# Kernel optimization log

Hardware: AMD Instinct MI355X
Metric: run time of the kernel (lower is better)

The kernel has to match this reference:

```python
import jax, jax.numpy as jnp
import numpy as np

N_NODES = 50000
N_EDGES = 1_600_000
F_IN = 128
F_OUT = 8
K_TAPS = 4
AVG_DEG = 32.0


def setup_inputs() -> dict:
    key = jax.random.key(0)
    k1, k2, k3, k4, k5 = jax.random.split(key, 5)
    x = jax.random.normal(k1, (N_NODES, F_IN), dtype=jnp.float32)
    gso_rows = jax.random.randint(k2, (N_EDGES,), 0, N_NODES, dtype=jnp.int32)
    gso_cols = jax.random.randint(k3, (N_EDGES,), 0, N_NODES, dtype=jnp.int32)
    gso_vals = jax.random.uniform(k4, (N_EDGES,), dtype=jnp.float32) / AVG_DEG
    # filterCoeff = randn(outFeat, filter_order) * 0.1 as in torch __init__
    coeff = jax.random.normal(k5, (F_OUT, K_TAPS), dtype=jnp.float32) * 0.1
    return {"x": x, "gso_rows": gso_rows, "gso_cols": gso_cols,
            "gso_vals": gso_vals, "coeff": coeff}


def reference(x, gso_rows, gso_cols, gso_vals, coeff):
    # Faithful to the torch code INCLUDING its carried-over SpMV state:
    # output feature o uses powers S^{1+o(K-1)} .. S^{o(K-1)+K} of x.
    F_out, K = coeff.shape
    N = x.shape[0]
    max_power = F_out * (K - 1) + 1  # highest S power needed

    def spmv(Z):  # S @ Z via edge-list gather + segment_sum scatter
        return jax.ops.segment_sum(gso_vals[:, None] * Z[gso_cols], gso_rows,
                                   num_segments=N)

    def step(Z, _):
        Zn = spmv(Z)
        return Zn, Zn.sum(axis=1)  # sum over in-features done up-front

    # s[p-1, n] = sum_f (S^p x)[n, f], for p = 1..max_power
    _, s = jax.lax.scan(step, x, None, length=max_power)  # (max_power, N)

    # power index (0-based into s) used by output o, tap i: o*(K-1) + i
    idx = jnp.arange(F_out)[:, None] * (K - 1) + jnp.arange(K)[None, :]  # (F_out, K)
    sg = s[idx]  # (F_out, K, N)
    y = jnp.einsum('ok,okn->no', coeff, sg)  # (N, F_out)
    return y
```

## Files before the change

kernel.cpp:

```cpp
#include <hip/hip_runtime.h>
#include <hip/hip_bf16.h>

#define N_NODES 50000
#define N_EDGES 1600000
#define F_IN    128
#define F_OUT   8
#define K_TAPS  4
#define MAX_POWER 25

#define NBLK    256
#define RPB     196
#define CHUNK   4096
#define NPART   391
#define ECAP_G  8192
#define ECAP_L  6912
#define CSB     800

#define FSTRIDE 16

__device__ inline int wave_incl_scan(int v, int lane) {
    #pragma unroll
    for (int off = 1; off < 64; off <<= 1) {
        int t = __shfl_up(v, off, 64);
        if (lane >= off) v += t;
    }
    return v;
}

__device__ inline void st_coh(float* p, float v) {
    __hip_atomic_store(p, v, __ATOMIC_RELAXED, __HIP_MEMORY_SCOPE_AGENT);
}

__global__ void partition_kernel(const int* __restrict__ rows,
                                 const int* __restrict__ cols,
                                 const float* __restrict__ vals,
                                 int* __restrict__ gcnt,
                                 int2* __restrict__ edges, int n_edges) {
    __shared__ int lhist[NBLK];
    __shared__ int lcur[NBLK];
    __shared__ int lbase[NBLK];
    __shared__ int2 stage[CHUNK];
    __shared__ unsigned char sbkt[CHUNK];
    __shared__ int wsum[4];
    int tid = threadIdx.x;
    int base = blockIdx.x * CHUNK;
    int cend = min(base + CHUNK, n_edges);

    lhist[tid] = 0;
    __syncthreads();
    for (int i = base + tid; i < cend; i += 256)
        atomicAdd(&lhist[rows[i] / RPB], 1);
    __syncthreads();

    int lane = tid & 63, wid = tid >> 6;
    int h = lhist[tid];
    int incl = wave_incl_scan(h, lane);
    if (lane == 63) wsum[wid] = incl;
    __syncthreads();
    int woff = 0;
    for (int w = 0; w < wid; ++w) woff += wsum[w];
    int excl = woff + incl - h;
    lcur[tid] = excl;
    if (h) {
        int g = atomicAdd(&gcnt[tid], h);
        lbase[tid] = tid * ECAP_G + g - excl;
    }
    __syncthreads();

    for (int i = base + tid; i < cend; i += 256) {
        int r = rows[i], c = cols[i];
        float v = vals[i];
        int b = r / RPB;
        int pos = atomicAdd(&lcur[b], 1);
        stage[pos] = make_int2(((r - b * RPB) << 16) | c, __float_as_int(v));
        sbkt[pos] = (unsigned char)b;
    }
    __syncthreads();

    int cn = cend - base;
    for (int i = tid; i < cn; i += 256) {
        int b = sbkt[i];
        int o = lbase[b] + i;
        if (o - b * ECAP_G < ECAP_G)
            edges[o] = stage[i];
    }
}

__device__ inline void gbar(int gen, int* __restrict__ flags) {
    __syncthreads();
    if (threadIdx.x == 0)
        __hip_atomic_store(&flags[blockIdx.x * FSTRIDE], gen,
                           __ATOMIC_RELAXED, __HIP_MEMORY_SCOPE_AGENT);
    if (threadIdx.x < NBLK) {
        while (__hip_atomic_load(&flags[threadIdx.x * FSTRIDE],
                                 __ATOMIC_RELAXED, __HIP_MEMORY_SCOPE_AGENT) < gen)
            __builtin_amdgcn_s_sleep(2);
    }
    __syncthreads();
}

__global__ __launch_bounds__(512, 1)
void chain_kernel(const int* __restrict__ gcnt,
                  const int2* __restrict__ edges,
                  const float* __restrict__ x,
                  const float* __restrict__ coeff,
                  float* __restrict__ u,
                  float* __restrict__ s,
                  float* __restrict__ y,
                  int* __restrict__ flags,
                  int n_nodes) {
    __shared__ int2  esort[ECAP_L];
    __shared__ int   chist[CSB];
    __shared__ int   ccur[CSB];
    __shared__ int   wsum8[8];
    __shared__ float acc[RPB];
    __shared__ float yacc[RPB * F_OUT];
    __shared__ float lcoeff[F_OUT * K_TAPS];

    int tid = threadIdx.x;
    int b = blockIdx.x;

    if (tid < RPB) acc[tid] = 0.f;
    for (int j = tid; j < RPB * F_OUT; j += 512) yacc[j] = 0.f;
    if (tid < F_OUT * K_TAPS) lcoeff[tid] = coeff[tid];

    int cnt = min(gcnt[b], ECAP_G);
    int cntl = min(cnt, ECAP_L);
    const int2* eb = edges + (size_t)b * ECAP_G;

    for (int i = tid; i < CSB; i += 512) chist[i] = 0;
    __syncthreads();
    if (cnt <= ECAP_L) {
        for (int i = tid; i < cnt; i += 512) {
            int2 e = eb[i];
            atomicAdd(&chist[(e.x & 0xFFFF) >> 6], 1);
        }
        __syncthreads();
        int lane = tid & 63, wid = tid >> 6;
        int b0 = 2 * tid;
        int h0 = (b0 < CSB) ? chist[b0] : 0;
        int h1 = (b0 + 1 < CSB) ? chist[b0 + 1] : 0;
        int ps = h0 + h1;
        int incl = wave_incl_scan(ps, lane);
        if (lane == 63) wsum8[wid] = incl;
        __syncthreads();
        int woff = 0;
        for (int w = 0; w < wid; ++w) woff += wsum8[w];
        int ex = woff + incl - ps;
        if (b0 < CSB) ccur[b0] = ex;
        if (b0 + 1 < CSB) ccur[b0 + 1] = ex + h0;
        __syncthreads();
        for (int i = tid; i < cnt; i += 512) {
            int2 e = eb[i];
            int pos = atomicAdd(&ccur[(e.x & 0xFFFF) >> 6], 1);
            esort[pos] = e;
        }
    } else {
        for (int i = tid; i < cntl; i += 512) esort[i] = eb[i];
    }

    {
        int lane = tid & 63;
        int wave = (b * 512 + tid) >> 6;
        int n_waves = NBLK * 8;
        for (int node = wave; node < n_nodes; node += n_waves) {
            const float2* xp = (const float2*)(x + (size_t)node * F_IN);
            float2 v = xp[lane];
            float sm = v.x + v.y;
            #pragma unroll
            for (int off = 32; off > 0; off >>= 1)
                sm += __shfl_down(sm, off, 64);
            if (lane == 0) st_coh(&u[node], sm);
        }
    }
    gbar(1, flags);

    for (int p = 0; p < MAX_POWER; ++p) {
        const float* __restrict__ src = (p == 0) ? u : s + (size_t)(p - 1) * n_nodes;
        float* dst = s + (size_t)p * n_nodes;

        int i = tid;
        for (; i + 3 * 512 < cntl; i += 4 * 512) {
            int2 e0 = esort[i];
            int2 e1 = esort[i + 512];
            int2 e2 = esort[i + 1024];
            int2 e3 = esort[i + 1536];
            float v0 = src[e0.x & 0xFFFF];
            float v1 = src[e1.x & 0xFFFF];
            float v2 = src[e2.x & 0xFFFF];
            float v3 = src[e3.x & 0xFFFF];
            atomicAdd(&acc[e0.x >> 16], __int_as_float(e0.y) * v0);
            atomicAdd(&acc[e1.x >> 16], __int_as_float(e1.y) * v1);
            atomicAdd(&acc[e2.x >> 16], __int_as_float(e2.y) * v2);
            atomicAdd(&acc[e3.x >> 16], __int_as_float(e3.y) * v3);
        }
        for (; i < cntl; i += 512) {
            int2 ev = esort[i];
            atomicAdd(&acc[ev.x >> 16], __int_as_float(ev.y) * src[ev.x & 0xFFFF]);
        }
        for (int k = ECAP_L + tid; k < cnt; k += 512) {
            int2 ev = eb[k];
            atomicAdd(&acc[ev.x >> 16], __int_as_float(ev.y) * src[ev.x & 0xFFFF]);
        }
        __syncthreads();

        if (tid < RPB) {
            int row = b * RPB + tid;
            float val = acc[tid];
            acc[tid] = 0.f;
            if (p < MAX_POWER - 1 && row < n_nodes) st_coh(&dst[row], val);
            #pragma unroll
            for (int o = 0; o < F_OUT; ++o) {
                int k = p - (K_TAPS - 1) * o;
                if (k >= 0 && k < K_TAPS)
                    yacc[tid * F_OUT + o] += lcoeff[o * K_TAPS + k] * val;
            }
        }
        if (p < MAX_POWER - 1)
            gbar(p + 2, flags);
    }

    __syncthreads();
    for (int j = tid; j < RPB * F_OUT; j += 512) {
        int row = b * RPB + (j >> 3);
        if (row < n_nodes) y[(size_t)row * F_OUT + (j & 7)] = yacc[j];
    }
}

extern "C" void kernel_launch(void* const* d_in, const int* in_sizes, int n_in,
                              void* d_out, int out_size, void* d_ws, size_t ws_size,
                              hipStream_t stream) {
    const float* x        = (const float*)d_in[0];
    const int*   gso_rows = (const int*)d_in[1];
    const int*   gso_cols = (const int*)d_in[2];
    const float* gso_vals = (const float*)d_in[3];
    const float* coeff    = (const float*)d_in[4];
    float* y = (float*)d_out;

    float* u     = (float*)d_ws;
    float* s     = u + N_NODES;
    int2*  edges = (int2*)(s + (size_t)MAX_POWER * N_NODES);
    int*   gcnt  = (int*)(edges + (size_t)NBLK * ECAP_G);
    int*   flags = gcnt + NBLK;

    size_t ctrl_ints = (size_t)NBLK + (size_t)NBLK * FSTRIDE;
    hipMemsetAsync(gcnt, 0, ctrl_ints * sizeof(int), stream);

    partition_kernel<<<NPART, 256, 0, stream>>>(
        gso_rows, gso_cols, gso_vals, gcnt, edges, N_EDGES);

    int n_nodes = N_NODES;
    void* args[] = { (void*)&gcnt, (void*)&edges, (void*)&x, (void*)&coeff,
                     (void*)&u, (void*)&s, (void*)&y, (void*)&flags,
                     (void*)&n_nodes };
    hipLaunchCooperativeKernel((void*)chain_kernel, dim3(NBLK), dim3(512),
                               args, 0, stream);
}
```

Before: 411.0 us.

## Use master-block grid barrier and keep per-block edges in registers

Replaces the all-to-all flag-polling grid barrier with a two-level scheme: block 0 polls every block's flag and then publishes a single generation word that the other blocks spin on. Each thread's share of sorted edges (up to 14) is preloaded once into registers, so the power loop issues all gathers before the LDS atomics instead of re-reading shared memory each iteration. The ECAP_L capacity grows slightly, and flag publication moves earlier so the yacc update overlaps the barrier wait. The costs are higher register pressure and an extra hop of latency through block 0 on every barrier.

```diff
diff --git a/kernel.cpp b/kernel.cpp
--- a/kernel.cpp
+++ b/kernel.cpp
@@ -9,11 +9,13 @@
 #define MAX_POWER 25
 
 #define NBLK    256
+#define NTHR    512
 #define RPB     196
 #define CHUNK   4096
 #define NPART   391
 #define ECAP_G  8192
-#define ECAP_L  6912
+#define ECAP_L  7168
+#define NITER   14
 #define CSB     800
 
 #define FSTRIDE 16
@@ -29,6 +31,12 @@
 
 __device__ inline void st_coh(float* p, float v) {
     __hip_atomic_store(p, v, __ATOMIC_RELAXED, __HIP_MEMORY_SCOPE_AGENT);
+}
+__device__ inline void st_coh_i(int* p, int v) {
+    __hip_atomic_store(p, v, __ATOMIC_RELAXED, __HIP_MEMORY_SCOPE_AGENT);
+}
+__device__ inline int ld_coh_i(const int* p) {
+    return __hip_atomic_load((int*)p, __ATOMIC_RELAXED, __HIP_MEMORY_SCOPE_AGENT);
 }
 
 __global__ void partition_kernel(const int* __restrict__ rows,
@@ -86,20 +94,7 @@
     }
 }
 
-__device__ inline void gbar(int gen, int* __restrict__ flags) {
-    __syncthreads();
-    if (threadIdx.x == 0)
-        __hip_atomic_store(&flags[blockIdx.x * FSTRIDE], gen,
-                           __ATOMIC_RELAXED, __HIP_MEMORY_SCOPE_AGENT);
-    if (threadIdx.x < NBLK) {
-        while (__hip_atomic_load(&flags[threadIdx.x * FSTRIDE],
-                                 __ATOMIC_RELAXED, __HIP_MEMORY_SCOPE_AGENT) < gen)
-            __builtin_amdgcn_s_sleep(2);
-    }
-    __syncthreads();
-}
-
-__global__ __launch_bounds__(512, 1)
+__global__ __launch_bounds__(NTHR, 1)
 void chain_kernel(const int* __restrict__ gcnt,
                   const int2* __restrict__ edges,
                   const float* __restrict__ x,
@@ -108,6 +103,7 @@
                   float* __restrict__ s,
                   float* __restrict__ y,
                   int* __restrict__ flags,
+                  int* __restrict__ gen_word,
                   int n_nodes) {
     __shared__ int2  esort[ECAP_L];
     __shared__ int   chist[CSB];
@@ -121,17 +117,16 @@
     int b = blockIdx.x;
 
     if (tid < RPB) acc[tid] = 0.f;
-    for (int j = tid; j < RPB * F_OUT; j += 512) yacc[j] = 0.f;
+    for (int j = tid; j < RPB * F_OUT; j += NTHR) yacc[j] = 0.f;
     if (tid < F_OUT * K_TAPS) lcoeff[tid] = coeff[tid];
 
     int cnt = min(gcnt[b], ECAP_G);
-    int cntl = min(cnt, ECAP_L);
     const int2* eb = edges + (size_t)b * ECAP_G;
 
-    for (int i = tid; i < CSB; i += 512) chist[i] = 0;
+    for (int i = tid; i < CSB; i += NTHR) chist[i] = 0;
     __syncthreads();
     if (cnt <= ECAP_L) {
-        for (int i = tid; i < cnt; i += 512) {
+        for (int i = tid; i < cnt; i += NTHR) {
             int2 e = eb[i];
             atomicAdd(&chist[(e.x & 0xFFFF) >> 6], 1);
         }
@@ -150,18 +145,34 @@
         if (b0 < CSB) ccur[b0] = ex;
         if (b0 + 1 < CSB) ccur[b0 + 1] = ex + h0;
         __syncthreads();
-        for (int i = tid; i < cnt; i += 512) {
+        for (int i = tid; i < cnt; i += NTHR) {
             int2 e = eb[i];
             int pos = atomicAdd(&ccur[(e.x & 0xFFFF) >> 6], 1);
             esort[pos] = e;
         }
+        __syncthreads();
     } else {
-        for (int i = tid; i < cntl; i += 512) esort[i] = eb[i];
+        int cl = min(cnt, ECAP_L);
+        for (int i = tid; i < cl; i += NTHR) esort[i] = eb[i];
+        __syncthreads();
+    }
+
+    int   ecol[NITER];
+    int   erow[NITER];
+    float eval[NITER];
+    int cntl = min(cnt, ECAP_L);
+    #pragma unroll
+    for (int j = 0; j < NITER; ++j) {
+        int idx = tid + j * NTHR;
+        int2 e = (idx < cntl) ? esort[idx] : make_int2(0, 0);
+        ecol[j] = e.x & 0xFFFF;
+        erow[j] = e.x >> 16;
+        eval[j] = __int_as_float(e.y);
     }
 
     {
         int lane = tid & 63;
-        int wave = (b * 512 + tid) >> 6;
+        int wave = (b * NTHR + tid) >> 6;
         int n_waves = NBLK * 8;
         for (int node = wave; node < n_nodes; node += n_waves) {
             const float2* xp = (const float2*)(x + (size_t)node * F_IN);
@@ -173,42 +184,43 @@
             if (lane == 0) st_coh(&u[node], sm);
         }
     }
-    gbar(1, flags);
+    __syncthreads();
+    if (tid == 0) st_coh_i(&flags[b * FSTRIDE], 1);
+    if (b == 0 && tid < NBLK)
+        while (ld_coh_i(&flags[tid * FSTRIDE]) < 1) __builtin_amdgcn_s_sleep(1);
+    __syncthreads();
+    if (b == 0 && tid == 0) st_coh_i(gen_word, 1);
+    if (tid == 0)
+        while (ld_coh_i(gen_word) < 1) __builtin_amdgcn_s_sleep(1);
+    __syncthreads();
 
     for (int p = 0; p < MAX_POWER; ++p) {
         const float* __restrict__ src = (p == 0) ? u : s + (size_t)(p - 1) * n_nodes;
         float* dst = s + (size_t)p * n_nodes;
 
-        int i = tid;
-        for (; i + 3 * 512 < cntl; i += 4 * 512) {
-            int2 e0 = esort[i];
-            int2 e1 = esort[i + 512];
-            int2 e2 = esort[i + 1024];
-            int2 e3 = esort[i + 1536];
-            float v0 = src[e0.x & 0xFFFF];
-            float v1 = src[e1.x & 0xFFFF];
-            float v2 = src[e2.x & 0xFFFF];
-            float v3 = src[e3.x & 0xFFFF];
-            atomicAdd(&acc[e0.x >> 16], __int_as_float(e0.y) * v0);
-            atomicAdd(&acc[e1.x >> 16], __int_as_float(e1.y) * v1);
-            atomicAdd(&acc[e2.x >> 16], __int_as_float(e2.y) * v2);
-            atomicAdd(&acc[e3.x >> 16], __int_as_float(e3.y) * v3);
-        }
-        for (; i < cntl; i += 512) {
-            int2 ev = esort[i];
-            atomicAdd(&acc[ev.x >> 16], __int_as_float(ev.y) * src[ev.x & 0xFFFF]);
-        }
-        for (int k = ECAP_L + tid; k < cnt; k += 512) {
+        float v[NITER];
+        #pragma unroll
+        for (int j = 0; j < NITER; ++j) v[j] = src[ecol[j]];
+        #pragma unroll
+        for (int j = 0; j < NITER; ++j)
+            atomicAdd(&acc[erow[j]], eval[j] * v[j]);
+        for (int k = ECAP_L + tid; k < cnt; k += NTHR) {
             int2 ev = eb[k];
             atomicAdd(&acc[ev.x >> 16], __int_as_float(ev.y) * src[ev.x & 0xFFFF]);
         }
         __syncthreads();
 
+        float val = (tid < RPB) ? acc[tid] : 0.f;
+        int row = b * RPB + tid;
+        bool last = (p == MAX_POWER - 1);
+        if (!last && tid < RPB && row < n_nodes) st_coh(&dst[row], val);
+
+        if (!last) {
+            __syncthreads();
+            if (tid == 0) st_coh_i(&flags[b * FSTRIDE], p + 2);
+        }
         if (tid < RPB) {
-            int row = b * RPB + tid;
-            float val = acc[tid];
             acc[tid] = 0.f;
-            if (p < MAX_POWER - 1 && row < n_nodes) st_coh(&dst[row], val);
             #pragma unroll
             for (int o = 0; o < F_OUT; ++o) {
                 int k = p - (K_TAPS - 1) * o;
@@ -216,12 +228,20 @@
                     yacc[tid * F_OUT + o] += lcoeff[o * K_TAPS + k] * val;
             }
         }
-        if (p < MAX_POWER - 1)
-            gbar(p + 2, flags);
-    }
-
-    __syncthreads();
-    for (int j = tid; j < RPB * F_OUT; j += 512) {
+        if (!last) {
+            if (b == 0 && tid < NBLK)
+                while (ld_coh_i(&flags[tid * FSTRIDE]) < p + 2)
+                    __builtin_amdgcn_s_sleep(1);
+            __syncthreads();
+            if (b == 0 && tid == 0) st_coh_i(gen_word, p + 2);
+            if (tid == 0)
+                while (ld_coh_i(gen_word) < p + 2) __builtin_amdgcn_s_sleep(1);
+            __syncthreads();
+        }
+    }
+
+    __syncthreads();
+    for (int j = tid; j < RPB * F_OUT; j += NTHR) {
         int row = b * RPB + (j >> 3);
         if (row < n_nodes) y[(size_t)row * F_OUT + (j & 7)] = yacc[j];
     }
@@ -242,8 +262,9 @@
     int2*  edges = (int2*)(s + (size_t)MAX_POWER * N_NODES);
     int*   gcnt  = (int*)(edges + (size_t)NBLK * ECAP_G);
     int*   flags = gcnt + NBLK;
-
-    size_t ctrl_ints = (size_t)NBLK + (size_t)NBLK * FSTRIDE;
+    int*   gen_word = flags + NBLK * FSTRIDE;
+
+    size_t ctrl_ints = (size_t)NBLK + (size_t)NBLK * FSTRIDE + 16;
     hipMemsetAsync(gcnt, 0, ctrl_ints * sizeof(int), stream);
 
     partition_kernel<<<NPART, 256, 0, stream>>>(
@@ -252,7 +273,7 @@
     int n_nodes = N_NODES;
     void* args[] = { (void*)&gcnt, (void*)&edges, (void*)&x, (void*)&coeff,
                      (void*)&u, (void*)&s, (void*)&y, (void*)&flags,
-                     (void*)&n_nodes };
-    hipLaunchCooperativeKernel((void*)chain_kernel, dim3(NBLK), dim3(512),
+                     (void*)&gen_word, (void*)&n_nodes };
+    hipLaunchCooperativeKernel((void*)chain_kernel, dim3(NBLK), dim3(NTHR),
                                args, 0, stream);
 }
```

Result: slower. 491.0 us (+19.5%).
